# Performance work log

Measured on AMD Instinct MI355X. Metric: run time of the kernel, lower is better.

The kernel has to match this reference:

```python
import jax, jax.numpy as jnp
import numpy as np

N_NODES = 100000


def _sage_conv(x, src, dst, W_l, b_l, W_r, n_nodes):
    # mean-aggregate neighbor features: messages flow src -> dst
    msg = x[src]                                              # [E, d]
    agg_sum = jax.ops.segment_sum(msg, dst, num_segments=n_nodes)   # [N, d]
    cnt = jax.ops.segment_sum(jnp.ones((src.shape[0],), x.dtype), dst,
                              num_segments=n_nodes)           # [N]
    agg = agg_sum / jnp.maximum(cnt, 1.0)[:, None]            # mean, 0 for isolated nodes
    return agg @ W_l + b_l + x @ W_r                          # lin_l(agg) + lin_r(x)


def setup_inputs() -> dict:
    key = jax.random.key(0)
    ks = jax.random.split(key, 8)
    in_c, hid_c, out_c = 64, 128, 64
    n_edges = 1000000
    x = jax.random.normal(ks[0], (N_NODES, in_c), dtype=jnp.float32)
    edge_index = jax.random.randint(ks[1], (2, n_edges), 0, N_NODES, dtype=jnp.int32)
    def glorot(k, shape):
        lim = float(np.sqrt(6.0 / (shape[0] + shape[1])))
        return jax.random.uniform(k, shape, jnp.float32, -lim, lim)
    return {
        "x": x,
        "edge_index": edge_index,
        "W_l1": glorot(ks[2], (in_c, hid_c)),
        "b_l1": jnp.zeros((hid_c,), jnp.float32),
        "W_r1": glorot(ks[3], (in_c, hid_c)),
        "W_l2": glorot(ks[4], (hid_c, out_c)),
        "b_l2": jnp.zeros((out_c,), jnp.float32),
        "W_r2": glorot(ks[5], (hid_c, out_c)),
    }


def reference(x, edge_index, W_l1, b_l1, W_r1, W_l2, b_l2, W_r2):
    src, dst = edge_index[0], edge_index[1]
    # eval mode: dropout(p=0.5) is identity
    h = _sage_conv(x, src, dst, W_l1, b_l1, W_r1, N_NODES)
    h = jax.nn.relu(h)
    out = _sage_conv(h, src, dst, W_l2, b_l2, W_r2, N_NODES)
    return out
```

## Files before the change

### kernel.cpp

```cpp
#include <hip/hip_runtime.h>


#define NPB 128
#define NBK 782
#define BCAP 1600

typedef __attribute__((ext_vector_type(8))) short bf16x8;
typedef __attribute__((ext_vector_type(4))) float f32x4;
typedef __attribute__((ext_vector_type(4))) int int4v;

__device__ __forceinline__ float bf2f(unsigned short u) {
  return __uint_as_float(((unsigned)u) << 16);
}
__device__ __forceinline__ unsigned short f2bf(float f) {
  unsigned x = __float_as_uint(f);
  x += 0x7fffu + ((x >> 16) & 1u);
  return (unsigned short)(x >> 16);
}

__global__ __launch_bounds__(256) void fused_misc(
    const float* __restrict__ x, unsigned short* __restrict__ xb, int total4,
    const float* __restrict__ Wl1, const float* __restrict__ Wr1,
    const float* __restrict__ Wl2, const float* __restrict__ Wr2,
    unsigned short* __restrict__ Wt1, unsigned short* __restrict__ Wcat,
    int* __restrict__ gcnt, int CB) {
  int b = blockIdx.x;
  if (b < CB) {
    int i = b * 256 + threadIdx.x;
    if (i < total4) {
      float4 v = ((const float4*)x)[i];
      ushort4 o;
      o.x = f2bf(v.x); o.y = f2bf(v.y); o.z = f2bf(v.z); o.w = f2bf(v.w);
      ((ushort4*)xb)[i] = o;
    }
  } else if (b < CB + 128) {
    int o = (b - CB) * 256 + threadIdx.x;
    if (o < 16384) {
      int m = o >> 13, rem = o & 8191;
      int col = rem >> 6, k = rem & 63;
      const float* W = m ? Wr1 : Wl1;
      Wt1[o] = f2bf(W[k * 128 + col]);
    } else {
      int o2 = o - 16384;
      int col = o2 >> 7, k = o2 & 127;
      float v = (col < 64) ? Wl2[k * 64 + col] : Wr2[k * 64 + col - 64];
      Wcat[o2] = f2bf(v);
    }
  } else {
    for (int i = threadIdx.x; i < NBK; i += 256) gcnt[i] = 0;
  }
}

__global__ __launch_bounds__(256) void bucketize(
    const int* __restrict__ src, const int* __restrict__ dst,
    int* __restrict__ gcnt, int* __restrict__ ebuf, int e) {
  __shared__ int lcnt[NBK], lbase[NBK];
  for (int i = threadIdx.x; i < NBK; i += 256) lcnt[i] = 0;
  __syncthreads();
  int pk[16], bk[16];
  int nv = 0;
  int base = blockIdx.x * 4096 + threadIdx.x * 4;
#pragma unroll
  for (int c = 0; c < 4; ++c) {
    int i = base + c * 1024;
    if (i + 4 <= e) {
      int4v sv = *(const int4v*)(src + i);
      int4v dv = *(const int4v*)(dst + i);
#pragma unroll
      for (int j = 0; j < 4; ++j) {
        bk[nv] = dv[j] >> 7;
        pk[nv] = ((dv[j] & 127) << 17) | sv[j];
        ++nv;
      }
    } else if (i < e) {
      for (int i2 = i; i2 < e; ++i2) {
        int dj = dst[i2], sj = src[i2];
        bk[nv] = dj >> 7;
        pk[nv] = ((dj & 127) << 17) | sj;
        ++nv;
      }
    }
  }
  for (int k = 0; k < nv; ++k) atomicAdd(&lcnt[bk[k]], 1);
  __syncthreads();
  for (int i = threadIdx.x; i < NBK; i += 256) {
    lbase[i] = atomicAdd(&gcnt[i], lcnt[i]);
    lcnt[i] = 0;
  }
  __syncthreads();
  for (int k = 0; k < nv; ++k) {
    int off = lbase[bk[k]] + atomicAdd(&lcnt[bk[k]], 1);
    if (off < BCAP) ebuf[bk[k] * BCAP + off] = pk[k];
  }
}

__global__ __launch_bounds__(256) void sort_write(
    const int* __restrict__ gcnt, const int* __restrict__ ebuf,
    int* __restrict__ srcS, int* __restrict__ nstart, int* __restrict__ ncnt,
    int n) {
  __shared__ int cnt[NPB], cur[NPB], st[NPB + 1], sorted[BCAP];
  int tid = threadIdx.x, lane = tid & 63, wid = tid >> 6;
  int b = blockIdx.x;
  if (tid < NPB) { cnt[tid] = 0; cur[tid] = 0; }
  __syncthreads();
  int ecnt = min(gcnt[b], BCAP);
  const int* eb = ebuf + b * BCAP;
  for (int i = tid; i < ecnt; i += 256) atomicAdd(&cnt[eb[i] >> 17], 1);
  __syncthreads();
  if (wid == 0) {
    int i0 = cnt[lane], i1 = cnt[64 + lane];
#pragma unroll
    for (int off = 1; off < 64; off <<= 1) {
      int u = __shfl_up(i0, off);
      if (lane >= off) i0 += u;
    }
    int t0 = __shfl(i0, 63);
#pragma unroll
    for (int off = 1; off < 64; off <<= 1) {
      int u = __shfl_up(i1, off);
      if (lane >= off) i1 += u;
    }
    st[lane + 1] = i0;
    st[64 + lane + 1] = t0 + i1;
    if (lane == 0) st[0] = 0;
  }
  __syncthreads();
  for (int i = tid; i < ecnt; i += 256) {
    int pk = eb[i];
    int dl = pk >> 17;
    int pos = st[dl] + atomicAdd(&cur[dl], 1);
    sorted[pos] = pk & 0x1FFFF;
  }
  __syncthreads();
  for (int i = tid; i < ecnt; i += 256) srcS[b * BCAP + i] = sorted[i];
  if (tid < NPB) {
    int node = b * NPB + tid;
    if (node < n) {
      nstart[node] = b * BCAP + st[tid];
      ncnt[node] = cnt[tid];
    }
  }
}

__device__ __forceinline__ void gather_node(
    const unsigned short* __restrict__ feat, const int* __restrict__ srcIdx,
    int s, int e, int lane, float* acc) {
  int lane8 = lane >> 3, ch8 = lane & 7;
  int d = e - s;
#pragma unroll
  for (int j = 0; j < 8; ++j) acc[j] = 0.f;
  if (d > 0) {
    int idx = srcIdx[min(s + lane, e - 1)];
    int nit = min((d + 7) >> 3, 8);
    bf16x8 c[8];
#pragma unroll
    for (int u = 0; u < 8; ++u) {
      if (u < nit) {
        int r = u * 8 + lane8;
        int sidx = __shfl(idx, min(r, d - 1));
        c[u] = *(const bf16x8*)(feat + (size_t)sidx * 64 + ch8 * 8);
      }
    }
#pragma unroll
    for (int u = 0; u < 8; ++u) {
      if (u < nit) {
        bool valid = (u * 8 + lane8) < d;
#pragma unroll
        for (int j = 0; j < 8; ++j)
          acc[j] += valid ? bf2f((unsigned short)c[u][j]) : 0.f;
      }
    }
    for (int b0 = 64; b0 < d; b0 += 64) {
      int idx2 = srcIdx[min(s + b0 + lane, e - 1)];
      int m = min(d - b0, 64);
      int nit2 = (m + 7) >> 3;
      for (int u = 0; u < nit2; ++u) {
        int r = u * 8 + lane8;
        int sidx = __shfl(idx2, min(r, m - 1));
        bf16x8 v = *(const bf16x8*)(feat + (size_t)sidx * 64 + ch8 * 8);
        bool valid = r < m;
#pragma unroll
        for (int j = 0; j < 8; ++j)
          acc[j] += valid ? bf2f((unsigned short)v[j]) : 0.f;
      }
    }
  }
#pragma unroll
  for (int m = 8; m < 64; m <<= 1) {
#pragma unroll
    for (int j = 0; j < 8; ++j) acc[j] += __shfl_xor(acc[j], m);
  }
}

__global__ __launch_bounds__(256) void agg_mean_fast(
    const unsigned short* __restrict__ feat, const int* __restrict__ nstart,
    const int* __restrict__ ncnt, const int* __restrict__ srcS,
    unsigned short* __restrict__ outp, int n) {
  int wid = threadIdx.x >> 6, lane = threadIdx.x & 63;
  int node = blockIdx.x * 4 + wid;
  if (node >= n) return;
  int s = nstart[node];
  int c = ncnt[node];
  float acc[8];
  gather_node(feat, srcS, s, s + c, lane, acc);
  float inv = 1.f / (float)max(c, 1);
  if (lane < 8) {
    bf16x8 o;
#pragma unroll
    for (int j = 0; j < 8; ++j) o[j] = (short)f2bf(acc[j] * inv);
    *(bf16x8*)(outp + (size_t)node * 64 + lane * 8) = o;
  }
}

__global__ __launch_bounds__(256) void agg_add_fast(
    const unsigned short* __restrict__ feat, const int* __restrict__ nstart,
    const int* __restrict__ ncnt, const int* __restrict__ srcS,
    float* __restrict__ outp, int n) {
  int wid = threadIdx.x >> 6, lane = threadIdx.x & 63;
  int node = blockIdx.x * 4 + wid;
  if (node >= n) return;
  int s = nstart[node];
  int c = ncnt[node];
  float acc[8];
  gather_node(feat, srcS, s, s + c, lane, acc);
  float inv = 1.f / (float)max(c, 1);
  if (lane < 8) {
    float4* op = (float4*)(outp + (size_t)node * 64 + lane * 8);
    float4 o0 = op[0], o1 = op[1];
    o0.x += acc[0] * inv; o0.y += acc[1] * inv;
    o0.z += acc[2] * inv; o0.w += acc[3] * inv;
    o1.x += acc[4] * inv; o1.y += acc[5] * inv;
    o1.z += acc[6] * inv; o1.w += acc[7] * inv;
    op[0] = o0; op[1] = o1;
  }
}

__global__ __launch_bounds__(256) void gemm1_mfma(
    const unsigned short* __restrict__ agg, const unsigned short* __restrict__ xb,
    const unsigned short* __restrict__ Wt1, const float* __restrict__ b1,
    unsigned short* __restrict__ h, int n) {
  __shared__ unsigned short sW[16384];
  int tid = threadIdx.x;
  int lane = tid & 63, wid = tid >> 6;
  int l15 = lane & 15, g = lane >> 4;
#pragma unroll
  for (int it = 0; it < 8; ++it) {
    int i = it * 256 + tid;
    int byte = i << 4;
    int col = (byte >> 7) & 127;
    int koff = (byte & 127) ^ ((col & 7) << 4);
    int dstb = (byte & ~127) | koff;
    bf16x8 v = *(const bf16x8*)(Wt1 + i * 8);
    *(bf16x8*)((char*)sW + dstb) = v;
  }
  float bj[8];
#pragma unroll
  for (int cb = 0; cb < 8; ++cb) bj[cb] = b1[cb * 16 + l15];
  __syncthreads();

  int rowbase = blockIdx.x * 128 + wid * 32;
  int r0 = rowbase + l15, r1 = r0 + 16;
  size_t cr0 = (size_t)min(r0, n - 1), cr1 = (size_t)min(r1, n - 1);

  f32x4 acc[2][8];
#pragma unroll
  for (int fr = 0; fr < 2; ++fr)
#pragma unroll
    for (int cb = 0; cb < 8; ++cb) acc[fr][cb] = (f32x4){0.f, 0.f, 0.f, 0.f};

#pragma unroll
  for (int m = 0; m < 2; ++m) {
    const char* base = m ? (const char*)xb : (const char*)agg;
#pragma unroll
    for (int s = 0; s < 2; ++s) {
      int ko = s * 64 + g * 16;
      bf16x8 a0 = *(const bf16x8*)(base + cr0 * 128 + ko);
      bf16x8 a1 = *(const bf16x8*)(base + cr1 * 128 + ko);
#pragma unroll
      for (int cb = 0; cb < 8; ++cb) {
        int col = cb * 16 + l15;
        int koff = ko ^ ((col & 7) << 4);
        bf16x8 b = *(const bf16x8*)((const char*)sW + m * 16384 + col * 128 + koff);
        acc[0][cb] = __builtin_amdgcn_mfma_f32_16x16x32_bf16(a0, b, acc[0][cb], 0, 0, 0);
        acc[1][cb] = __builtin_amdgcn_mfma_f32_16x16x32_bf16(a1, b, acc[1][cb], 0, 0, 0);
      }
    }
  }
#pragma unroll
  for (int fr = 0; fr < 2; ++fr) {
    int rb = rowbase + fr * 16 + g * 4;
#pragma unroll
    for (int r = 0; r < 4; ++r) {
      int row = rb + r;
      if (row < n) {
        unsigned short* hp = h + (size_t)row * 128 + l15;
#pragma unroll
        for (int cb = 0; cb < 8; ++cb) {
          float v = fmaxf(acc[fr][cb][r] + bj[cb], 0.f);
          hp[cb * 16] = f2bf(v);
        }
      }
    }
  }
}

__global__ __launch_bounds__(256) void gemm2_mfma(
    const unsigned short* __restrict__ h, const unsigned short* __restrict__ Wcat,
    const float* __restrict__ b2, unsigned short* __restrict__ t,
    float* __restrict__ outp, int n) {
  __shared__ unsigned short sW[16384];
  int tid = threadIdx.x;
  int lane = tid & 63, wid = tid >> 6;
  int l15 = lane & 15, g = lane >> 4;
#pragma unroll
  for (int it = 0; it < 8; ++it) {
    int i = it * 256 + tid;
    int byte = i << 4;
    int col = byte >> 8;
    int koff = (byte & 255) ^ ((col & 15) << 4);
    int dstb = (byte & ~255) | koff;
    bf16x8 v = *(const bf16x8*)(Wcat + i * 8);
    *(bf16x8*)((char*)sW + dstb) = v;
  }
  float bj[4];
#pragma unroll
  for (int cb = 0; cb < 4; ++cb) bj[cb] = b2[cb * 16 + l15];
  __syncthreads();

  int rowbase = blockIdx.x * 128 + wid * 32;
  int r0 = rowbase + l15, r1 = r0 + 16;
  size_t cr0 = (size_t)min(r0, n - 1), cr1 = (size_t)min(r1, n - 1);

  f32x4 acc[2][8];
#pragma unroll
  for (int fr = 0; fr < 2; ++fr)
#pragma unroll
    for (int cb = 0; cb < 8; ++cb) acc[fr][cb] = (f32x4){0.f, 0.f, 0.f, 0.f};

  const char* hb = (const char*)h;
#pragma unroll
  for (int s = 0; s < 4; ++s) {
    int ko = s * 64 + g * 16;
    bf16x8 a0 = *(const bf16x8*)(hb + cr0 * 256 + ko);
    bf16x8 a1 = *(const bf16x8*)(hb + cr1 * 256 + ko);
#pragma unroll
    for (int cb = 0; cb < 8; ++cb) {
      int col = cb * 16 + l15;
      int koff = ko ^ ((col & 15) << 4);
      bf16x8 b = *(const bf16x8*)((const char*)sW + col * 256 + koff);
      acc[0][cb] = __builtin_amdgcn_mfma_f32_16x16x32_bf16(a0, b, acc[0][cb], 0, 0, 0);
      acc[1][cb] = __builtin_amdgcn_mfma_f32_16x16x32_bf16(a1, b, acc[1][cb], 0, 0, 0);
    }
  }
#pragma unroll
  for (int fr = 0; fr < 2; ++fr) {
    int rb = rowbase + fr * 16 + g * 4;
#pragma unroll
    for (int r = 0; r < 4; ++r) {
      int row = rb + r;
      if (row < n) {
#pragma unroll
        for (int cb = 0; cb < 4; ++cb)
          t[(size_t)row * 64 + cb * 16 + l15] = f2bf(acc[fr][cb][r]);
#pragma unroll
        for (int cb = 0; cb < 4; ++cb)
          outp[(size_t)row * 64 + cb * 16 + l15] = acc[fr][cb + 4][r] + bj[cb];
      }
    }
  }
}

extern "C" void kernel_launch(void* const* d_in, const int* in_sizes, int n_in,
                              void* d_out, int out_size, void* d_ws, size_t ws_size,
                              hipStream_t stream) {
  const float* x   = (const float*)d_in[0];
  const int*   ei  = (const int*)d_in[1];
  const float* Wl1 = (const float*)d_in[2];
  const float* b1  = (const float*)d_in[3];
  const float* Wr1 = (const float*)d_in[4];
  const float* Wl2 = (const float*)d_in[5];
  const float* b2  = (const float*)d_in[6];
  const float* Wr2 = (const float*)d_in[7];
  float* out = (float*)d_out;

  const int n = in_sizes[0] / 64;
  const int e = in_sizes[1] / 2;
  const int* src = ei;
  const int* dst = ei + e;

  char* ws = (char*)d_ws;
  size_t off = 0;
  auto take = [&](size_t bytes) { void* p = ws + off; off = (off + bytes + 255) & ~(size_t)255; return p; };
  int*            gcnt   = (int*)take((size_t)NBK * 4);
  int*            ebuf   = (int*)take((size_t)NBK * BCAP * 4);
  int*            srcS   = (int*)take((size_t)NBK * BCAP * 4);
  int*            nstart = (int*)take((size_t)n * 4);
  int*            ncnt   = (int*)take((size_t)n * 4);
  unsigned short* xb     = (unsigned short*)take((size_t)n * 64 * 2);
  unsigned short* agg1b  = (unsigned short*)take((size_t)n * 64 * 2);
  unsigned short* h      = (unsigned short*)take((size_t)n * 128 * 2);
  unsigned short* t      = agg1b;
  unsigned short* Wt1    = (unsigned short*)take(16384 * 2);
  unsigned short* Wcat   = (unsigned short*)take(16384 * 2);

  const int NTILE = (n + 127) / 128;
  const int total4 = n * 64 / 4;
  const int CB = (total4 + 255) / 256;

  fused_misc<<<CB + 128 + 1, 256, 0, stream>>>(x, xb, total4,
                                               Wl1, Wr1, Wl2, Wr2, Wt1, Wcat,
                                               gcnt, CB);
  bucketize<<<(e + 4095) / 4096, 256, 0, stream>>>(src, dst, gcnt, ebuf, e);
  sort_write<<<NBK, 256, 0, stream>>>(gcnt, ebuf, srcS, nstart, ncnt, n);

  agg_mean_fast<<<(n + 3) / 4, 256, 0, stream>>>(xb, nstart, ncnt, srcS, agg1b, n);
  gemm1_mfma<<<NTILE, 256, 0, stream>>>(agg1b, xb, Wt1, b1, h, n);

  gemm2_mfma<<<NTILE, 256, 0, stream>>>(h, Wcat, b2, t, out, n);
  agg_add_fast<<<(n + 3) / 4, 256, 0, stream>>>(t, nstart, ncnt, srcS, out, n);
}
```

Measured before the change: 136.5 us.

## Gather two nodes per wavefront with degree padded to multiples of four

The aggregation kernels now give each half-wavefront (32 lanes) its own destination node, so one wavefront gathers two nodes at once. Per-node edge lists in the CSR are padded to a multiple of four with a sentinel index that points to an added zero row in the feature buffers. This removes the per-element validity masks and the clamped index logic. The cost is a larger sorted-index buffer, extra zero rows, and some wasted loads of padding rows. It also adds a risk that a bucket overflows its 2048-slot capacity when padding is added.

```diff
diff --git a/kernel.cpp b/kernel.cpp
--- a/kernel.cpp
+++ b/kernel.cpp
@@ -3,7 +3,8 @@
 
 #define NPB 128
 #define NBK 782
-#define BCAP 1600
+#define BCAP_E 1600
+#define BCAP_S 2048
 
 typedef __attribute__((ext_vector_type(8))) short bf16x8;
 typedef __attribute__((ext_vector_type(4))) float f32x4;
@@ -23,7 +24,8 @@
     const float* __restrict__ Wl1, const float* __restrict__ Wr1,
     const float* __restrict__ Wl2, const float* __restrict__ Wr2,
     unsigned short* __restrict__ Wt1, unsigned short* __restrict__ Wcat,
-    int* __restrict__ gcnt, int CB) {
+    int* __restrict__ gcnt, unsigned short* __restrict__ agg1b,
+    int n, int CB) {
   int b = blockIdx.x;
   if (b < CB) {
     int i = b * 256 + threadIdx.x;
@@ -48,6 +50,10 @@
     }
   } else {
     for (int i = threadIdx.x; i < NBK; i += 256) gcnt[i] = 0;
+    if (threadIdx.x < 32) {
+      ((unsigned*)(xb + (size_t)n * 64))[threadIdx.x] = 0;
+      ((unsigned*)(agg1b + (size_t)n * 64))[threadIdx.x] = 0;
+    }
   }
 }
 
@@ -90,7 +96,7 @@
   __syncthreads();
   for (int k = 0; k < nv; ++k) {
     int off = lbase[bk[k]] + atomicAdd(&lcnt[bk[k]], 1);
-    if (off < BCAP) ebuf[bk[k] * BCAP + off] = pk[k];
+    if (off < BCAP_E) ebuf[bk[k] * BCAP_E + off] = pk[k];
   }
 }
 
@@ -98,17 +104,17 @@
     const int* __restrict__ gcnt, const int* __restrict__ ebuf,
     int* __restrict__ srcS, int* __restrict__ nstart, int* __restrict__ ncnt,
     int n) {
-  __shared__ int cnt[NPB], cur[NPB], st[NPB + 1], sorted[BCAP];
+  __shared__ int cnt[NPB], cur[NPB], st[NPB + 1], sorted[BCAP_S];
   int tid = threadIdx.x, lane = tid & 63, wid = tid >> 6;
   int b = blockIdx.x;
   if (tid < NPB) { cnt[tid] = 0; cur[tid] = 0; }
   __syncthreads();
-  int ecnt = min(gcnt[b], BCAP);
-  const int* eb = ebuf + b * BCAP;
+  int ecnt = min(gcnt[b], BCAP_E);
+  const int* eb = ebuf + b * BCAP_E;
   for (int i = tid; i < ecnt; i += 256) atomicAdd(&cnt[eb[i] >> 17], 1);
   __syncthreads();
   if (wid == 0) {
-    int i0 = cnt[lane], i1 = cnt[64 + lane];
+    int i0 = (cnt[lane] + 3) & ~3, i1 = (cnt[64 + lane] + 3) & ~3;
 #pragma unroll
     for (int off = 1; off < 64; off <<= 1) {
       int u = __shfl_up(i0, off);
@@ -129,64 +135,70 @@
     int pk = eb[i];
     int dl = pk >> 17;
     int pos = st[dl] + atomicAdd(&cur[dl], 1);
-    sorted[pos] = pk & 0x1FFFF;
-  }
-  __syncthreads();
-  for (int i = tid; i < ecnt; i += 256) srcS[b * BCAP + i] = sorted[i];
+    if (pos < BCAP_S) sorted[pos] = pk & 0x1FFFF;
+  }
+  __syncthreads();
+  if (tid < NPB) {
+    int c = cnt[tid], p = (c + 3) & ~3;
+    int base = st[tid];
+    for (int k = c; k < p; ++k)
+      if (base + k < BCAP_S) sorted[base + k] = n;
+  }
+  __syncthreads();
+  int total = min(st[NPB], BCAP_S);
+  for (int i = tid; i < total; i += 256) srcS[b * BCAP_S + i] = sorted[i];
   if (tid < NPB) {
     int node = b * NPB + tid;
     if (node < n) {
-      nstart[node] = b * BCAP + st[tid];
+      nstart[node] = b * BCAP_S + st[tid];
       ncnt[node] = cnt[tid];
     }
   }
 }
 
-__device__ __forceinline__ void gather_node(
-    const unsigned short* __restrict__ feat, const int* __restrict__ srcIdx,
-    int s, int e, int lane, float* acc) {
-  int lane8 = lane >> 3, ch8 = lane & 7;
-  int d = e - s;
+__device__ __forceinline__ void gather2(
+    const unsigned short* __restrict__ feat, const int* __restrict__ srcS,
+    int s, int dpad, int lane, float* acc) {
+  int half32 = lane & 32;
+  int hlane = lane & 31;
+  int g = hlane >> 3;
+  int ch8 = lane & 7;
 #pragma unroll
   for (int j = 0; j < 8; ++j) acc[j] = 0.f;
-  if (d > 0) {
-    int idx = srcIdx[min(s + lane, e - 1)];
-    int nit = min((d + 7) >> 3, 8);
-    bf16x8 c[8];
+  int nit = dpad >> 2;
+  int nitw = max(nit, __shfl_xor(nit, 32));
+  int idx = srcS[s + hlane];
+  bf16x8 c[8];
+#pragma unroll
+  for (int u = 0; u < 8; ++u) {
+    if (u < nitw) {
+      int r = u * 4 + g;
+      int sidx = __shfl(idx, half32 + r);
+      if (u < nit) c[u] = *(const bf16x8*)(feat + (size_t)sidx * 64 + ch8 * 8);
+    }
+  }
+#pragma unroll
+  for (int u = 0; u < 8; ++u) {
+    if (u < nitw && u < nit) {
+#pragma unroll
+      for (int j = 0; j < 8; ++j) acc[j] += bf2f((unsigned short)c[u][j]);
+    }
+  }
+  for (int b0 = 32; b0 < dpad; b0 += 32) {
+    int idx2 = srcS[s + b0 + hlane];
 #pragma unroll
     for (int u = 0; u < 8; ++u) {
-      if (u < nit) {
-        int r = u * 8 + lane8;
-        int sidx = __shfl(idx, min(r, d - 1));
-        c[u] = *(const bf16x8*)(feat + (size_t)sidx * 64 + ch8 * 8);
-      }
-    }
-#pragma unroll
-    for (int u = 0; u < 8; ++u) {
-      if (u < nit) {
-        bool valid = (u * 8 + lane8) < d;
-#pragma unroll
-        for (int j = 0; j < 8; ++j)
-          acc[j] += valid ? bf2f((unsigned short)c[u][j]) : 0.f;
-      }
-    }
-    for (int b0 = 64; b0 < d; b0 += 64) {
-      int idx2 = srcIdx[min(s + b0 + lane, e - 1)];
-      int m = min(d - b0, 64);
-      int nit2 = (m + 7) >> 3;
-      for (int u = 0; u < nit2; ++u) {
-        int r = u * 8 + lane8;
-        int sidx = __shfl(idx2, min(r, m - 1));
+      int r = u * 4 + g;
+      if (b0 + r < dpad) {
+        int sidx = __shfl(idx2, half32 + r);
         bf16x8 v = *(const bf16x8*)(feat + (size_t)sidx * 64 + ch8 * 8);
-        bool valid = r < m;
-#pragma unroll
-        for (int j = 0; j < 8; ++j)
-          acc[j] += valid ? bf2f((unsigned short)v[j]) : 0.f;
-      }
-    }
-  }
-#pragma unroll
-  for (int m = 8; m < 64; m <<= 1) {
+#pragma unroll
+        for (int j = 0; j < 8; ++j) acc[j] += bf2f((unsigned short)v[j]);
+      }
+    }
+  }
+#pragma unroll
+  for (int m = 8; m < 32; m <<= 1) {
 #pragma unroll
     for (int j = 0; j < 8; ++j) acc[j] += __shfl_xor(acc[j], m);
   }
@@ -196,19 +208,22 @@
     const unsigned short* __restrict__ feat, const int* __restrict__ nstart,
     const int* __restrict__ ncnt, const int* __restrict__ srcS,
     unsigned short* __restrict__ outp, int n) {
-  int wid = threadIdx.x >> 6, lane = threadIdx.x & 63;
-  int node = blockIdx.x * 4 + wid;
-  if (node >= n) return;
-  int s = nstart[node];
-  int c = ncnt[node];
+  int lane = threadIdx.x & 63, wid = threadIdx.x >> 6;
+  int half = lane >> 5;
+  int node = (blockIdx.x * 4 + wid) * 2 + half;
+  bool live = node < n;
+  int cn = live ? node : n - 1;
+  int s = nstart[cn];
+  int c = ncnt[cn];
+  int dpad = (c + 3) & ~3;
   float acc[8];
-  gather_node(feat, srcS, s, s + c, lane, acc);
+  gather2(feat, srcS, s, dpad, lane, acc);
   float inv = 1.f / (float)max(c, 1);
-  if (lane < 8) {
+  if ((lane & 31) < 8 && live) {
     bf16x8 o;
 #pragma unroll
     for (int j = 0; j < 8; ++j) o[j] = (short)f2bf(acc[j] * inv);
-    *(bf16x8*)(outp + (size_t)node * 64 + lane * 8) = o;
+    *(bf16x8*)(outp + (size_t)node * 64 + (lane & 7) * 8) = o;
   }
 }
 
@@ -216,16 +231,19 @@
     const unsigned short* __restrict__ feat, const int* __restrict__ nstart,
     const int* __restrict__ ncnt, const int* __restrict__ srcS,
     float* __restrict__ outp, int n) {
-  int wid = threadIdx.x >> 6, lane = threadIdx.x & 63;
-  int node = blockIdx.x * 4 + wid;
-  if (node >= n) return;
-  int s = nstart[node];
-  int c = ncnt[node];
+  int lane = threadIdx.x & 63, wid = threadIdx.x >> 6;
+  int half = lane >> 5;
+  int node = (blockIdx.x * 4 + wid) * 2 + half;
+  bool live = node < n;
+  int cn = live ? node : n - 1;
+  int s = nstart[cn];
+  int c = ncnt[cn];
+  int dpad = (c + 3) & ~3;
   float acc[8];
-  gather_node(feat, srcS, s, s + c, lane, acc);
+  gather2(feat, srcS, s, dpad, lane, acc);
   float inv = 1.f / (float)max(c, 1);
-  if (lane < 8) {
-    float4* op = (float4*)(outp + (size_t)node * 64 + lane * 8);
+  if ((lane & 31) < 8 && live) {
+    float4* op = (float4*)(outp + (size_t)node * 64 + (lane & 7) * 8);
     float4 o0 = op[0], o1 = op[1];
     o0.x += acc[0] * inv; o0.y += acc[1] * inv;
     o0.z += acc[2] * inv; o0.w += acc[3] * inv;
@@ -392,12 +410,12 @@
   size_t off = 0;
   auto take = [&](size_t bytes) { void* p = ws + off; off = (off + bytes + 255) & ~(size_t)255; return p; };
   int*            gcnt   = (int*)take((size_t)NBK * 4);
-  int*            ebuf   = (int*)take((size_t)NBK * BCAP * 4);
-  int*            srcS   = (int*)take((size_t)NBK * BCAP * 4);
+  int*            ebuf   = (int*)take((size_t)NBK * BCAP_E * 4);
+  int*            srcS   = (int*)take((size_t)NBK * BCAP_S * 4 + 256);
   int*            nstart = (int*)take((size_t)n * 4);
   int*            ncnt   = (int*)take((size_t)n * 4);
-  unsigned short* xb     = (unsigned short*)take((size_t)n * 64 * 2);
-  unsigned short* agg1b  = (unsigned short*)take((size_t)n * 64 * 2);
+  unsigned short* xb     = (unsigned short*)take(((size_t)n + 1) * 64 * 2);
+  unsigned short* agg1b  = (unsigned short*)take(((size_t)n + 1) * 64 * 2);
   unsigned short* h      = (unsigned short*)take((size_t)n * 128 * 2);
   unsigned short* t      = agg1b;
   unsigned short* Wt1    = (unsigned short*)take(16384 * 2);
@@ -409,13 +427,13 @@
 
   fused_misc<<<CB + 128 + 1, 256, 0, stream>>>(x, xb, total4,
                                                Wl1, Wr1, Wl2, Wr2, Wt1, Wcat,
-                                               gcnt, CB);
+                                               gcnt, agg1b, n, CB);
   bucketize<<<(e + 4095) / 4096, 256, 0, stream>>>(src, dst, gcnt, ebuf, e);
   sort_write<<<NBK, 256, 0, stream>>>(gcnt, ebuf, srcS, nstart, ncnt, n);
 
-  agg_mean_fast<<<(n + 3) / 4, 256, 0, stream>>>(xb, nstart, ncnt, srcS, agg1b, n);
+  agg_mean_fast<<<(n + 7) / 8, 256, 0, stream>>>(xb, nstart, ncnt, srcS, agg1b, n);
   gemm1_mfma<<<NTILE, 256, 0, stream>>>(agg1b, xb, Wt1, b1, h, n);
 
   gemm2_mfma<<<NTILE, 256, 0, stream>>>(h, Wcat, b2, t, out, n);
-  agg_add_fast<<<(n + 3) / 4, 256, 0, stream>>>(t, nstart, ncnt, srcS, out, n);
-}
+  agg_add_fast<<<(n + 7) / 8, 256, 0, stream>>>(t, nstart, ncnt, srcS, out, n);
+}
```

Measured after the change: 115.9 us (median of 2 runs). -15.1%, faster.
